# Kernel optimization log

Hardware: AMD Instinct MI355X
Metric: run time of the kernel (lower is better)

Reference implementation:

```python
import jax, jax.numpy as jnp
import numpy as np

B, S, D, H = 2, 2048, 1024, 16
HD = D // H


def setup_inputs() -> dict:
    key = jax.random.key(0)
    ks = jax.random.split(key, 12)
    sc = 0.02
    inp = {
        "q": jax.random.normal(ks[0], (B, S, D), jnp.float32),
        "k": jax.random.normal(ks[1], (B, S, D), jnp.float32),
        "v": jax.random.normal(ks[2], (B, S, D), jnp.float32),
        # causal mask, broadcastable to [B,H,S,S]; 0 => masked
        "mask": jnp.tril(jnp.ones((S, S), jnp.int32))[None, None],
        "Wq": jax.random.normal(ks[3], (D, D), jnp.float32) * sc,
        "bq": jnp.zeros((D,), jnp.float32),
        "Wk": jax.random.normal(ks[4], (D, D), jnp.float32) * sc,
        "bk": jnp.zeros((D,), jnp.float32),
        "Wv": jax.random.normal(ks[5], (D, D), jnp.float32) * sc,
        "bv": jnp.zeros((D,), jnp.float32),
        "Wf": jax.random.normal(ks[6], (D, D), jnp.float32) * sc,
        "bf": jnp.zeros((D,), jnp.float32),
    }
    return inp


def reference(q, k, v, mask, Wq, bq, Wk, bk, Wv, bv, Wf, bf):
    b = q.shape[0]
    # projections (torch Linear: x @ W.T + b)
    qh = (q @ Wq.T + bq).reshape(b, -1, H, HD).transpose(0, 2, 1, 3)  # [B,H,S,HD]
    kh = (k @ Wk.T + bk).reshape(b, -1, H, HD).transpose(0, 2, 1, 3)
    vh = (v @ Wv.T + bv).reshape(b, -1, H, HD).transpose(0, 2, 1, 3)
    scores = jnp.einsum("bhqd,bhkd->bhqk", qh, kh) / jnp.sqrt(jnp.float32(HD))
    scores = jnp.where(mask == 0, jnp.float32(-1e9), scores)
    attn = jax.nn.softmax(scores, axis=-1)
    x = jnp.einsum("bhqk,bhkd->bhqd", attn, vh)  # [B,H,S,HD]
    x = x.transpose(0, 2, 1, 3).reshape(b, -1, D)
    return x @ Wf.T + bf
```

## Files before the change

kernel.cpp:

```cpp
#include <hip/hip_runtime.h>

typedef __attribute__((ext_vector_type(4))) float f32x4;
typedef __attribute__((ext_vector_type(8))) short bf16x8;
typedef unsigned short u16;
typedef unsigned int u32;

#define QSCALE 0.18033688011112042f

__device__ __forceinline__ u16 f2bf(float f) {
  union { float f; u32 u; } v; v.f = f;
  u32 r = v.u + 0x7fffu + ((v.u >> 16) & 1u);
  return (u16)(r >> 16);
}

__device__ __forceinline__ u32 cvtpk(float a, float b) {
  u32 r;
  asm("v_cvt_pk_bf16_f32 %0, %1, %2" : "=v"(r) : "v"(a), "v"(b));
  return r;
}

__device__ __forceinline__ void gl_lds16(const u16* g, u16* l) {
  __builtin_amdgcn_global_load_lds((const __attribute__((address_space(1))) u32*)g,
                                   (__attribute__((address_space(3))) u32*)l, 16, 0, 0);
}

__global__ __launch_bounds__(256) void conv_kernel(
    const float* __restrict__ q, const float* __restrict__ k, const float* __restrict__ v,
    const float* __restrict__ wq, const float* __restrict__ wk, const float* __restrict__ wv,
    const float* __restrict__ wf, u16* __restrict__ dst)
{
  size_t i = ((size_t)blockIdx.x * 256 + threadIdx.x) * 8;
  const float* src; size_t off;
  if (i < ((size_t)3 << 22)) {
    int a = (int)(i >> 22);
    src = (a == 0) ? q : ((a == 1) ? k : v);
    off = i & ((1u << 22) - 1);
  } else {
    size_t j = i - ((size_t)3 << 22);
    int a = (int)(j >> 20);
    src = (a == 0) ? wq : ((a == 1) ? wk : ((a == 2) ? wv : wf));
    off = j & ((1u << 20) - 1);
  }
  float4 x0 = *reinterpret_cast<const float4*>(src + off);
  float4 x1 = *reinterpret_cast<const float4*>(src + off + 4);
  u32 o[4] = {cvtpk(x0.x, x0.y), cvtpk(x0.z, x0.w), cvtpk(x1.x, x1.y), cvtpk(x1.z, x1.w)};
  *reinterpret_cast<uint4*>(dst + i) = *reinterpret_cast<const uint4*>(o);
}

struct GArg {
  const u16* X; const u16* W; const float* bias; void* out; int mode; float scale;
};

template<int BM>
__global__ __launch_bounds__(256) void gemm_bf(GArg a0, GArg a1, GArg a2) {
  constexpr int K = 1024, N = 1024;
  constexpr int WNw = (BM == 128) ? 2 : 4;
  constexpr int NI  = (128 / WNw) / 16;
  constexpr int CA  = BM / 32;
  __shared__ __align__(16) u16 lA[BM * 64];
  __shared__ __align__(16) u16 lB[128 * 64];
  GArg a = (blockIdx.z == 0) ? a0 : ((blockIdx.z == 1) ? a1 : a2);
  const int m0 = blockIdx.x * BM, n0 = blockIdx.y * 128;
  const int tid = threadIdx.x, w = tid >> 6, lane = tid & 63;
  const int lr = lane & 15, lg = lane >> 4;
  const int wm = (w / WNw) * 64, wn = (w % WNw) * (128 / WNw);
  const int lrow8 = lane >> 3, lc = lane & 7;
  const int schunk = (lc ^ lrow8) * 8;

  f32x4 acc[4][NI] = {};

  for (int kt = 0; kt < K; kt += 64) {
    #pragma unroll
    for (int c = 0; c < CA; ++c) {
      int row = w * (BM / 4) + c * 8 + lrow8;
      gl_lds16(a.X + (size_t)(m0 + row) * K + kt + schunk, &lA[(w * (BM / 4) + c * 8) * 64]);
    }
    #pragma unroll
    for (int c = 0; c < 4; ++c) {
      int row = w * 32 + c * 8 + lrow8;
      gl_lds16(a.W + (size_t)(n0 + row) * K + kt + schunk, &lB[(w * 32 + c * 8) * 64]);
    }
    __syncthreads();
    #pragma unroll
    for (int h = 0; h < 2; ++h) {
      bf16x8 af[4], bfv[NI];
      #pragma unroll
      for (int i = 0; i < 4; ++i) {
        int r = wm + i * 16 + lr;
        af[i] = *reinterpret_cast<const bf16x8*>(&lA[r * 64 + (((h * 4 + lg) ^ (r & 7)) * 8)]);
      }
      #pragma unroll
      for (int i = 0; i < NI; ++i) {
        int r = wn + i * 16 + lr;
        bfv[i] = *reinterpret_cast<const bf16x8*>(&lB[r * 64 + (((h * 4 + lg) ^ (r & 7)) * 8)]);
      }
      __builtin_amdgcn_s_setprio(1);
      #pragma unroll
      for (int mi = 0; mi < 4; ++mi)
        #pragma unroll
        for (int ni = 0; ni < NI; ++ni)
          acc[mi][ni] = __builtin_amdgcn_mfma_f32_16x16x32_bf16(af[mi], bfv[ni], acc[mi][ni], 0, 0, 0);
      __builtin_amdgcn_s_setprio(0);
    }
    __syncthreads();
  }

  #pragma unroll
  for (int mi = 0; mi < 4; ++mi) {
    #pragma unroll
    for (int ni = 0; ni < NI; ++ni) {
      int col = n0 + wn + ni * 16 + lr;
      float bv = a.bias[col];
      #pragma unroll
      for (int r = 0; r < 4; ++r) {
        int row = m0 + wm + mi * 16 + lg * 4 + r;
        float val = (acc[mi][ni][r] + bv) * a.scale;
        if (a.mode == 2) {
          ((float*)a.out)[(size_t)row * N + col] = val;
        } else {
          int b = row >> 11, s = row & 2047, hh = col >> 6, hd = col & 63;
          u16* O = (u16*)a.out;
          if (a.mode == 0) O[((size_t)(b * 16 + hh) * 2048 + s) * 64 + hd] = f2bf(val);
          else             O[((size_t)(b * 16 + hh) * 64 + hd) * 2048 + s] = f2bf(val);
        }
      }
    }
  }
}

template<int IN_BF16, int OUT_MODE>
__global__ __launch_bounds__(256) void gemm_legacy(
    const void* __restrict__ Xv, const float* __restrict__ W,
    const float* __restrict__ bias, void* __restrict__ Outv, float scale)
{
  constexpr int N = 1024, K = 1024;
  __shared__ __align__(16) u16 lA[128 * 32];
  __shared__ __align__(16) u16 lB[128 * 32];
  const int n0 = blockIdx.x * 128, m0 = blockIdx.y * 128;
  const int tid = threadIdx.x;
  const int w = tid >> 6, lane = tid & 63, lr = lane & 15, lg = lane >> 4;
  const int wm = (w >> 1) * 64, wn = (w & 1) * 64;
  f32x4 acc[4][4] = {};
  for (int kt = 0; kt < K; kt += 32) {
    #pragma unroll
    for (int it = 0; it < 4; ++it) {
      int idx = it * 256 + tid, row = idx >> 3, c4 = idx & 7;
      float4 xv = *reinterpret_cast<const float4*>(&W[(size_t)(n0 + row) * K + kt + c4 * 4]);
      u16* dst = &lB[row * 32 + c4 * 4];
      dst[0] = f2bf(xv.x); dst[1] = f2bf(xv.y); dst[2] = f2bf(xv.z); dst[3] = f2bf(xv.w);
    }
    if (IN_BF16 == 0) {
      const float* X = (const float*)Xv;
      #pragma unroll
      for (int it = 0; it < 4; ++it) {
        int idx = it * 256 + tid, row = idx >> 3, c4 = idx & 7;
        float4 xv = *reinterpret_cast<const float4*>(&X[(size_t)(m0 + row) * K + kt + c4 * 4]);
        u16* dst = &lA[row * 32 + c4 * 4];
        dst[0] = f2bf(xv.x); dst[1] = f2bf(xv.y); dst[2] = f2bf(xv.z); dst[3] = f2bf(xv.w);
      }
    } else {
      const u16* X = (const u16*)Xv;
      #pragma unroll
      for (int it = 0; it < 2; ++it) {
        int idx = it * 256 + tid, row = idx >> 2, c = idx & 3;
        *reinterpret_cast<uint4*>(&lA[row * 32 + c * 8]) =
            *reinterpret_cast<const uint4*>(&X[(size_t)(m0 + row) * K + kt + c * 8]);
      }
    }
    __syncthreads();
    bf16x8 af[4], bfr[4];
    #pragma unroll
    for (int i = 0; i < 4; ++i) {
      af[i]  = *reinterpret_cast<const bf16x8*>(&lA[(wm + i * 16 + lr) * 32 + lg * 8]);
      bfr[i] = *reinterpret_cast<const bf16x8*>(&lB[(wn + i * 16 + lr) * 32 + lg * 8]);
    }
    #pragma unroll
    for (int mi = 0; mi < 4; ++mi)
      #pragma unroll
      for (int ni = 0; ni < 4; ++ni)
        acc[mi][ni] = __builtin_amdgcn_mfma_f32_16x16x32_bf16(af[mi], bfr[ni], acc[mi][ni], 0, 0, 0);
    __syncthreads();
  }
  #pragma unroll
  for (int mi = 0; mi < 4; ++mi)
    #pragma unroll
    for (int ni = 0; ni < 4; ++ni) {
      int col = n0 + wn + ni * 16 + lr;
      float bv = bias[col];
      #pragma unroll
      for (int r = 0; r < 4; ++r) {
        int row = m0 + wm + mi * 16 + lg * 4 + r;
        float val = (acc[mi][ni][r] + bv) * scale;
        if (OUT_MODE == 2) {
          ((float*)Outv)[(size_t)row * N + col] = val;
        } else {
          int b = row >> 11, s = row & 2047, h = col >> 6, hd = col & 63;
          u16* O = (u16*)Outv;
          if (OUT_MODE == 0) O[((size_t)(b * 16 + h) * 2048 + s) * 64 + hd] = f2bf(val);
          else               O[((size_t)(b * 16 + h) * 64 + hd) * 2048 + s] = f2bf(val);
        }
      }
    }
}


__device__ __forceinline__ void seg_step4(
    const bf16x8* aq, f32x4* oacc, float& ls,
    const u16* lK, const u16* lV, char* pwb,
    bool diag, int col0, int qv, int lr, int lg, bf16x8 ones)
{
  const int cs = lr & 7;
  f32x4 sc[4];
  #pragma unroll
  for (int nf = 0; nf < 4; ++nf) {
    const u16* kr = &lK[(nf * 16 + lr) * 64];
    bf16x8 k0 = *reinterpret_cast<const bf16x8*>(&kr[(lg ^ cs) * 8]);
    bf16x8 k1 = *reinterpret_cast<const bf16x8*>(&kr[((4 + lg) ^ cs) * 8]);
    f32x4 z = {};
    __builtin_amdgcn_s_setprio(1);
    z = __builtin_amdgcn_mfma_f32_16x16x32_bf16(k0, aq[0], z, 0, 0, 0);
    z = __builtin_amdgcn_mfma_f32_16x16x32_bf16(k1, aq[1], z, 0, 0, 0);
    __builtin_amdgcn_s_setprio(0);
    sc[nf] = z;
  }
  if (diag) {
    #pragma unroll
    for (int nf = 0; nf < 4; ++nf)
      #pragma unroll
      for (int r = 0; r < 4; ++r)
        if ((col0 + nf * 16 + lg * 4 + r) > qv) sc[nf][r] = -1e30f;
  }
  #pragma unroll
  for (int nf = 0; nf < 4; ++nf) {
    float p0 = exp2f(sc[nf][0]), p1 = exp2f(sc[nf][1]);
    float p2 = exp2f(sc[nf][2]), p3 = exp2f(sc[nf][3]);
    uint2 pr;
    pr.x = cvtpk(p0, p1);
    pr.y = cvtpk(p2, p3);
    *reinterpret_cast<uint2*>(pwb + lr * 128 + ((32 * nf + 8 * lg) ^ (cs << 4))) = pr;
  }
  bf16x8 pb0 = *reinterpret_cast<const bf16x8*>(pwb + lr * 128 + 16 * (lg ^ cs));
  bf16x8 pb1 = *reinterpret_cast<const bf16x8*>(pwb + lr * 128 + 16 * ((4 + lg) ^ cs));
  f32x4 rs = {};
  rs = __builtin_amdgcn_mfma_f32_16x16x32_bf16(ones, pb0, rs, 0, 0, 0);
  rs = __builtin_amdgcn_mfma_f32_16x16x32_bf16(ones, pb1, rs, 0, 0, 0);
  ls += rs[0];
  #pragma unroll
  for (int df = 0; df < 4; ++df) {
    const u16* vr = &lV[(df * 16 + lr) * 64];
    bf16x8 v0 = *reinterpret_cast<const bf16x8*>(&vr[(lg ^ cs) * 8]);
    bf16x8 v1 = *reinterpret_cast<const bf16x8*>(&vr[((4 + lg) ^ cs) * 8]);
    __builtin_amdgcn_s_setprio(1);
    oacc[df] = __builtin_amdgcn_mfma_f32_16x16x32_bf16(v0, pb0, oacc[df], 0, 0, 0);
    oacc[df] = __builtin_amdgcn_mfma_f32_16x16x32_bf16(v1, pb1, oacc[df], 0, 0, 0);
    __builtin_amdgcn_s_setprio(0);
  }
}

__global__ __launch_bounds__(256) void attn_kernel7(
    const u16* __restrict__ Qh, const u16* __restrict__ Kh,
    const u16* __restrict__ Vt, u16* __restrict__ Oa)
{
  __shared__ __align__(16) u16 lK[2][64 * 64];
  __shared__ __align__(16) u16 lV[2][64 * 64];
  __shared__ __align__(16) u16 lP[4][2][16 * 64];
  const int bh = blockIdx.x, x = blockIdx.y;
  const int b = bh >> 4, h = bh & 15;
  const int tA = x, tB = 31 - x;
  const u16* Qb = Qh + (size_t)bh * 2048 * 64;
  const u16* Kb = Kh + (size_t)bh * 2048 * 64;
  const u16* Vb = Vt + (size_t)bh * 64 * 2048;
  const int tid = threadIdx.x, w = tid >> 6, lane = tid & 63;
  const int lr = lane & 15, lg = lane >> 4;
  const int lrow8 = lane >> 3, lc = lane & 7;
  const int schunk = (lc ^ lrow8) * 8;
  char* pwbB = (char*)lP[w][0];
  char* pwbA = (char*)lP[w][1];

  bf16x8 ones;
  #pragma unroll
  for (int j = 0; j < 8; ++j) ones[j] = (short)0x3F80;

  bf16x8 aqA[2], aqB[2];
  {
    int qrA = tA * 64 + w * 16 + lr;
    int qrB = tB * 64 + w * 16 + lr;
    aqA[0] = *reinterpret_cast<const bf16x8*>(&Qb[(size_t)qrA * 64 + lg * 8]);
    aqA[1] = *reinterpret_cast<const bf16x8*>(&Qb[(size_t)qrA * 64 + 32 + lg * 8]);
    aqB[0] = *reinterpret_cast<const bf16x8*>(&Qb[(size_t)qrB * 64 + lg * 8]);
    aqB[1] = *reinterpret_cast<const bf16x8*>(&Qb[(size_t)qrB * 64 + 32 + lg * 8]);
  }
  f32x4 oA[4] = {}, oB[4] = {};
  float lsA = 0.f, lsB = 0.f;
  const int rowgA = tA * 64 + w * 16, rowgB = tB * 64 + w * 16;
  const int qvA = rowgA + lr, qvB = rowgB + lr;

  const int nkt = tB + 1;
  int cur = 0;

  #pragma unroll
  for (int c = 0; c < 2; ++c) {
    int row = w * 16 + c * 8 + lrow8;
    gl_lds16(Kb + (size_t)row * 64 + schunk, &lK[0][(w * 16 + c * 8) * 64]);
    gl_lds16(Vb + (size_t)row * 2048 + schunk, &lV[0][(w * 16 + c * 8) * 64]);
  }
  __syncthreads();

  for (int kt = 0; kt < nkt; ++kt) {
    if (kt + 1 < nkt) {
      #pragma unroll
      for (int c = 0; c < 2; ++c) {
        int row = w * 16 + c * 8 + lrow8;
        gl_lds16(Kb + (size_t)((kt + 1) * 64 + row) * 64 + schunk, &lK[cur ^ 1][(w * 16 + c * 8) * 64]);
        gl_lds16(Vb + (size_t)row * 2048 + (kt + 1) * 64 + schunk, &lV[cur ^ 1][(w * 16 + c * 8) * 64]);
      }
    }
    seg_step4(aqB, oB, lsB, lK[cur], lV[cur], pwbB, kt == tB, kt * 64, qvB, lr, lg, ones);
    if (kt <= tA)
      seg_step4(aqA, oA, lsA, lK[cur], lV[cur], pwbA, kt == tA, kt * 64, qvA, lr, lg, ones);
    if (kt + 1 < nkt) __syncthreads();
    cur ^= 1;
  }

  float invA = 1.0f / lsA, invB = 1.0f / lsB;
  #pragma unroll
  for (int df = 0; df < 4; ++df) {
    uint2 pa, pb;
    pa.x = cvtpk(oA[df][0] * invA, oA[df][1] * invA);
    pa.y = cvtpk(oA[df][2] * invA, oA[df][3] * invA);
    *reinterpret_cast<uint2*>(&Oa[(size_t)(b * 2048 + qvA) * 1024 + h * 64 + df * 16 + lg * 4]) = pa;
    pb.x = cvtpk(oB[df][0] * invB, oB[df][1] * invB);
    pb.y = cvtpk(oB[df][2] * invB, oB[df][3] * invB);
    *reinterpret_cast<uint2*>(&Oa[(size_t)(b * 2048 + qvB) * 1024 + h * 64 + df * 16 + lg * 4]) = pb;
  }
}

extern "C" void kernel_launch(void* const* d_in, const int* in_sizes, int n_in,
                              void* d_out, int out_size, void* d_ws, size_t ws_size,
                              hipStream_t stream) {
  const float* q  = (const float*)d_in[0];
  const float* k  = (const float*)d_in[1];
  const float* v  = (const float*)d_in[2];
  const float* Wq = (const float*)d_in[4];
  const float* bq = (const float*)d_in[5];
  const float* Wk = (const float*)d_in[6];
  const float* bk = (const float*)d_in[7];
  const float* Wv = (const float*)d_in[8];
  const float* bv = (const float*)d_in[9];
  const float* Wf = (const float*)d_in[10];
  const float* bf = (const float*)d_in[11];

  if (ws_size >= ((size_t)64 << 20)) {
    u16* wsb = (u16*)d_ws;
    u16* qb  = wsb;
    u16* kb  = wsb + (1u << 22);
    u16* vb  = wsb + ((size_t)2 << 22);
    u16* wqb = wsb + ((size_t)3 << 22);
    u16* wkb = wqb + (1u << 20);
    u16* wvb = wkb + (1u << 20);
    u16* wfb = wvb + (1u << 20);
    u16* Qh  = wsb + ((size_t)1 << 24);
    u16* Kh  = Qh + (1u << 22);
    u16* Vt  = Kh + (1u << 22);
    u16* Oa  = Vt + (1u << 22);

    conv_kernel<<<8192, 256, 0, stream>>>(q, k, v, Wq, Wk, Wv, Wf, wsb);

    GArg gq{qb, wqb, bq, Qh, 0, QSCALE};
    GArg gk{kb, wkb, bk, Kh, 0, 1.0f};
    GArg gv{vb, wvb, bv, Vt, 1, 1.0f};
    gemm_bf<128><<<dim3(32, 8, 3), 256, 0, stream>>>(gq, gk, gv);

    attn_kernel7<<<dim3(32, 16), 256, 0, stream>>>(Qh, Kh, Vt, Oa);

    GArg gf{Oa, wfb, bf, d_out, 2, 1.0f};
    gemm_bf<64><<<dim3(64, 8, 1), 256, 0, stream>>>(gf, gf, gf);
  } else {
    u16* Qh = (u16*)d_ws;
    u16* Kh = Qh + (size_t)4096 * 1024;
    u16* Vt = Kh + (size_t)4096 * 1024;
    u16* Oa = Vt + (size_t)4096 * 1024;
    dim3 gg(8, 32), gb(256);
    gemm_legacy<0, 0><<<gg, gb, 0, stream>>>(q, Wq, bq, Qh, QSCALE);
    gemm_legacy<0, 0><<<gg, gb, 0, stream>>>(k, Wk, bk, Kh, 1.0f);
    gemm_legacy<0, 1><<<gg, gb, 0, stream>>>(v, Wv, bv, Vt, 1.0f);
    attn_kernel7<<<dim3(32, 16), gb, 0, stream>>>(Qh, Kh, Vt, Oa);
    gemm_legacy<1, 2><<<gg, gb, 0, stream>>>(Oa, Wf, bf, (float*)d_out, 1.0f);
  }
}
```

Baseline: 115.7 us.

## Replace paired causal Q-tile blocks with one Q-tile per block, heaviest first

The attention kernel stops pairing a short and a long causal query tile in each block and gives every block a single 64-row query tile, doubling the grid to 1024 blocks. Block y is mapped to tile 31-y, so the tiles with the most key tiles launch first, aiming for better load balance and occupancy with fewer registers and less LDS per block. The cost is that each K/V tile is no longer shared by two query tiles, so global loads of K/V roughly rise relative to compute.

```diff
diff --git a/kernel.cpp b/kernel.cpp
--- a/kernel.cpp
+++ b/kernel.cpp
@@ -257,16 +257,16 @@
   }
 }
 
-__global__ __launch_bounds__(256) void attn_kernel7(
+__global__ __launch_bounds__(256) void attn_kernel8(
     const u16* __restrict__ Qh, const u16* __restrict__ Kh,
     const u16* __restrict__ Vt, u16* __restrict__ Oa)
 {
   __shared__ __align__(16) u16 lK[2][64 * 64];
   __shared__ __align__(16) u16 lV[2][64 * 64];
-  __shared__ __align__(16) u16 lP[4][2][16 * 64];
-  const int bh = blockIdx.x, x = blockIdx.y;
+  __shared__ __align__(16) u16 lP[4][16 * 64];
+  const int bh = blockIdx.x;
+  const int t = 31 - blockIdx.y;
   const int b = bh >> 4, h = bh & 15;
-  const int tA = x, tB = 31 - x;
   const u16* Qb = Qh + (size_t)bh * 2048 * 64;
   const u16* Kb = Kh + (size_t)bh * 2048 * 64;
   const u16* Vb = Vt + (size_t)bh * 64 * 2048;
@@ -274,28 +274,23 @@
   const int lr = lane & 15, lg = lane >> 4;
   const int lrow8 = lane >> 3, lc = lane & 7;
   const int schunk = (lc ^ lrow8) * 8;
-  char* pwbB = (char*)lP[w][0];
-  char* pwbA = (char*)lP[w][1];
+  char* pwb = (char*)lP[w];
 
   bf16x8 ones;
   #pragma unroll
   for (int j = 0; j < 8; ++j) ones[j] = (short)0x3F80;
 
-  bf16x8 aqA[2], aqB[2];
+  bf16x8 aq[2];
   {
-    int qrA = tA * 64 + w * 16 + lr;
-    int qrB = tB * 64 + w * 16 + lr;
-    aqA[0] = *reinterpret_cast<const bf16x8*>(&Qb[(size_t)qrA * 64 + lg * 8]);
-    aqA[1] = *reinterpret_cast<const bf16x8*>(&Qb[(size_t)qrA * 64 + 32 + lg * 8]);
-    aqB[0] = *reinterpret_cast<const bf16x8*>(&Qb[(size_t)qrB * 64 + lg * 8]);
-    aqB[1] = *reinterpret_cast<const bf16x8*>(&Qb[(size_t)qrB * 64 + 32 + lg * 8]);
-  }
-  f32x4 oA[4] = {}, oB[4] = {};
-  float lsA = 0.f, lsB = 0.f;
-  const int rowgA = tA * 64 + w * 16, rowgB = tB * 64 + w * 16;
-  const int qvA = rowgA + lr, qvB = rowgB + lr;
-
-  const int nkt = tB + 1;
+    int qrow = t * 64 + w * 16 + lr;
+    aq[0] = *reinterpret_cast<const bf16x8*>(&Qb[(size_t)qrow * 64 + lg * 8]);
+    aq[1] = *reinterpret_cast<const bf16x8*>(&Qb[(size_t)qrow * 64 + 32 + lg * 8]);
+  }
+  f32x4 oacc[4] = {};
+  float ls = 0.f;
+  const int qv = t * 64 + w * 16 + lr;
+
+  const int nkt = t + 1;
   int cur = 0;
 
   #pragma unroll
@@ -315,23 +310,18 @@
         gl_lds16(Vb + (size_t)row * 2048 + (kt + 1) * 64 + schunk, &lV[cur ^ 1][(w * 16 + c * 8) * 64]);
       }
     }
-    seg_step4(aqB, oB, lsB, lK[cur], lV[cur], pwbB, kt == tB, kt * 64, qvB, lr, lg, ones);
-    if (kt <= tA)
-      seg_step4(aqA, oA, lsA, lK[cur], lV[cur], pwbA, kt == tA, kt * 64, qvA, lr, lg, ones);
+    seg_step4(aq, oacc, ls, lK[cur], lV[cur], pwb, kt == t, kt * 64, qv, lr, lg, ones);
     if (kt + 1 < nkt) __syncthreads();
     cur ^= 1;
   }
 
-  float invA = 1.0f / lsA, invB = 1.0f / lsB;
+  float inv = 1.0f / ls;
   #pragma unroll
   for (int df = 0; df < 4; ++df) {
-    uint2 pa, pb;
-    pa.x = cvtpk(oA[df][0] * invA, oA[df][1] * invA);
-    pa.y = cvtpk(oA[df][2] * invA, oA[df][3] * invA);
-    *reinterpret_cast<uint2*>(&Oa[(size_t)(b * 2048 + qvA) * 1024 + h * 64 + df * 16 + lg * 4]) = pa;
-    pb.x = cvtpk(oB[df][0] * invB, oB[df][1] * invB);
-    pb.y = cvtpk(oB[df][2] * invB, oB[df][3] * invB);
-    *reinterpret_cast<uint2*>(&Oa[(size_t)(b * 2048 + qvB) * 1024 + h * 64 + df * 16 + lg * 4]) = pb;
+    uint2 pa;
+    pa.x = cvtpk(oacc[df][0] * inv, oacc[df][1] * inv);
+    pa.y = cvtpk(oacc[df][2] * inv, oacc[df][3] * inv);
+    *reinterpret_cast<uint2*>(&Oa[(size_t)(b * 2048 + qv) * 1024 + h * 64 + df * 16 + lg * 4]) = pa;
   }
 }
 
@@ -371,7 +361,7 @@
     GArg gv{vb, wvb, bv, Vt, 1, 1.0f};
     gemm_bf<128><<<dim3(32, 8, 3), 256, 0, stream>>>(gq, gk, gv);
 
-    attn_kernel7<<<dim3(32, 16), 256, 0, stream>>>(Qh, Kh, Vt, Oa);
+    attn_kernel8<<<dim3(32, 32), 256, 0, stream>>>(Qh, Kh, Vt, Oa);
 
     GArg gf{Oa, wfb, bf, d_out, 2, 1.0f};
     gemm_bf<64><<<dim3(64, 8, 1), 256, 0, stream>>>(gf, gf, gf);
@@ -384,7 +374,7 @@
     gemm_legacy<0, 0><<<gg, gb, 0, stream>>>(q, Wq, bq, Qh, QSCALE);
     gemm_legacy<0, 0><<<gg, gb, 0, stream>>>(k, Wk, bk, Kh, 1.0f);
     gemm_legacy<0, 1><<<gg, gb, 0, stream>>>(v, Wv, bv, Vt, 1.0f);
-    attn_kernel7<<<dim3(32, 16), gb, 0, stream>>>(Qh, Kh, Vt, Oa);
+    attn_kernel8<<<dim3(32, 32), gb, 0, stream>>>(Qh, Kh, Vt, Oa);
     gemm_legacy<1, 2><<<gg, gb, 0, stream>>>(Oa, Wf, bf, (float*)d_out, 1.0f);
   }
 }
```

Measured after the change: 112.3 us. -3.0%, faster.
